# Optimization experiments

Measured on AMD Instinct MI355X. Metric: run time of the kernel, lower is better.

The kernel has to match this reference:

```python
import jax, jax.numpy as jnp
import numpy as np

# Dimensions (match init_kwargs / input_specs)
N = 50000      # num_nodes
R = 16         # num_relations
B = 8          # num_bases
DIN = 128      # indim
DOUT = 128     # outdim
NNZ = 1_600_000  # nonzeros in block-sparse relational adjacency A (N x R*N)


def setup_inputs() -> dict:
    key = jax.random.key(0)
    k0, k1, k2, k3, k4, k5 = jax.random.split(key, 6)
    X = jax.random.normal(k0, (N, DIN), dtype=jnp.float32)
    # COO representation of sparse A: rows in [0, N), cols in [0, R*N)
    A_rows = jax.random.randint(k1, (NNZ,), 0, N, dtype=jnp.int64)
    A_cols = jax.random.randint(k2, (NNZ,), 0, R * N, dtype=jnp.int64)
    A_vals = jax.random.uniform(k3, (NNZ,), dtype=jnp.float32)
    # Basis-decomposed relation weights (xavier-ish scale)
    weight_F = jax.random.normal(k4, (B, DIN, DOUT), dtype=jnp.float32) * 0.05
    weight_F_comp = jax.random.normal(k5, (R, B), dtype=jnp.float32) * 0.3
    return {"X": X, "A_rows": A_rows, "A_cols": A_cols, "A_vals": A_vals,
            "weight_F": weight_F, "weight_F_comp": weight_F_comp}


def reference(X, A_rows, A_cols, A_vals, weight_F, weight_F_comp):
    # Basis decomposition: per-relation weights W_F[r] = sum_b comp[r,b] * basis[b]
    W_F = jnp.einsum('rb,bij->rij', weight_F_comp, weight_F)          # (R, DIN, DOUT)
    # Per-relation feature transform: X @ W_F[r] for all r
    FW_F = jnp.einsum('nj,rjk->rnk', X, W_F)                          # (R, N, DOUT)
    FW_F = FW_F.reshape(R * N, DOUT)                                  # (R*N, DOUT)
    # Sparse-dense matmul A @ FW_F via gather + weighted segment-sum
    gathered = A_vals[:, None] * FW_F[A_cols]                          # (NNZ, DOUT)
    AFW_F = jax.ops.segment_sum(gathered, A_rows, num_segments=N)     # (N, DOUT)
    return AFW_F
```

## Files before the change

### kernel.cpp

```cpp
#include <hip/hip_runtime.h>

typedef unsigned int   uint32;
typedef unsigned short ushort16;

#define NN       50000
#define RR       16
#define BB       8
#define DIN      128
#define DOUT     128
#define K2       1024
#define NNZ_C    1600000
#define NBUCK    196
#define EPB      4096
#define NBLK_E   391

typedef short  short8  __attribute__((ext_vector_type(8)));
typedef float  floatx4 __attribute__((ext_vector_type(4)));
typedef float  float2v __attribute__((ext_vector_type(2)));

__device__ __forceinline__ ushort16 f2bf(float f) {
    uint32 u = __float_as_uint(f);
    u += 0x7fffu + ((u >> 16) & 1u);
    return (ushort16)(u >> 16);
}

__device__ __forceinline__ float bf2f(ushort16 h) {
    return __uint_as_float(((uint32)h) << 16);
}

__device__ __forceinline__ uint32 pack_bf16(float a, float b) {
    uint32 ua = __float_as_uint(a) + 0x8000u;
    uint32 ub = __float_as_uint(b) + 0x8000u;
    return __builtin_amdgcn_perm(ub, ua, 0x07060302);
}

__device__ __forceinline__ void gload16(const void* g, void* l) {
    __builtin_amdgcn_global_load_lds(
        (const __attribute__((address_space(1))) uint32*)g,
        (__attribute__((address_space(3))) uint32*)l, 16, 0, 0);
}

__global__ void build_bst_kernel(const float* __restrict__ basis,
                                 ushort16* __restrict__ Bst) {
    int idx  = blockIdx.x * 256 + threadIdx.x;
    int jout = idx >> 10;
    int bk   = idx & 1023;
    Bst[idx] = f2bf(basis[(size_t)bk * DOUT + jout]);
}

__global__ void cvt_x_kernel(const float* __restrict__ X,
                             uint32* __restrict__ XD) {
    int d = blockIdx.x * 256 + threadIdx.x;
    float2 f = *(const float2*)(X + (size_t)d * 2);
    XD[d] = pack_bf16(f.x, f.y);
}

__global__ void histB_kernel(const int* __restrict__ rows,
                             int* __restrict__ counts) {
    __shared__ int h[NBUCK];
    int tid = threadIdx.x;
    if (tid < NBUCK) h[tid] = 0;
    __syncthreads();
    int base_e = blockIdx.x * EPB;
#pragma unroll
    for (int it = 0; it < 16; ++it) {
        int e = base_e + it * 256 + tid;
        if (e < NNZ_C) atomicAdd(&h[rows[e] >> 8], 1);
    }
    __syncthreads();
    if (tid < NBUCK && h[tid]) atomicAdd(&counts[tid], h[tid]);
}

__global__ void scanB_kernel(const int* __restrict__ counts,
                             int* __restrict__ bucket_start,
                             int* __restrict__ cursor) {
    __shared__ int tmp[256];
    int tid = threadIdx.x;
    int v = (tid < NBUCK) ? counts[tid] : 0;
    tmp[tid] = v;
    __syncthreads();
#pragma unroll
    for (int off = 1; off < 256; off <<= 1) {
        int t = (tid >= off) ? tmp[tid - off] : 0;
        __syncthreads();
        tmp[tid] += t;
        __syncthreads();
    }
    if (tid < NBUCK) {
        bucket_start[tid + 1] = tmp[tid];
        cursor[tid] = tmp[tid] - v;
        if (tid == 0) bucket_start[0] = 0;
    }
}

__global__ __launch_bounds__(256) void scatterB_kernel(
        const int* __restrict__ rows,
        const int* __restrict__ cols,
        const float* __restrict__ vals,
        int* __restrict__ cursor,
        uint2* __restrict__ es2) {
    __shared__ int h[NBUCK], gbase[NBUCK], lcur[NBUCK];
    int tid = threadIdx.x;
    if (tid < NBUCK) { h[tid] = 0; lcur[tid] = 0; }
    __syncthreads();

    int    rowv[16];
    uint32 pkx[16];
    float  vv[16];
    int base_e = blockIdx.x * EPB;
#pragma unroll
    for (int it = 0; it < 16; ++it) {
        int e = base_e + it * 256 + tid;
        if (e < NNZ_C) {
            int row = rows[e];
            int col = cols[e];
            int r   = (int)((uint32)col / (uint32)NN);
            int c   = col - r * NN;
            rowv[it] = row;
            pkx[it]  = (uint32)c | ((uint32)(((row & 255) << 4) | r) << 16);
            vv[it]   = vals[e];
            atomicAdd(&h[row >> 8], 1);
        } else rowv[it] = -1;
    }
    __syncthreads();
    if (tid < NBUCK && h[tid] > 0)
        gbase[tid] = atomicAdd(&cursor[tid], h[tid]);
    __syncthreads();
#pragma unroll
    for (int it = 0; it < 16; ++it) {
        if (rowv[it] >= 0) {
            int b   = rowv[it] >> 8;
            int pos = gbase[b] + atomicAdd(&lcur[b], 1);
            es2[pos] = make_uint2(pkx[it], __float_as_uint(vv[it]));
        }
    }
}

__global__ __launch_bounds__(256) void sortB_kernel(
        const uint2* __restrict__ es2,
        const int* __restrict__ bucket_start,
        uint2* __restrict__ es,
        int* __restrict__ ks) {
    __shared__ int h[4096];
    __shared__ int cur[4096];
    __shared__ int tmp[256];
    int b    = blockIdx.x;
    int tid  = threadIdx.x;
    int base = bucket_start[b];
    int n    = bucket_start[b + 1] - base;

#pragma unroll
    for (int j = 0; j < 16; ++j) h[j * 256 + tid] = 0;
    __syncthreads();
    for (int i = tid; i < n; i += 256) {
        uint2 p = es2[base + i];
        atomicAdd(&h[(p.x >> 16) & 0xfffu], 1);
    }
    __syncthreads();

    int run = 0;
    int loc[16];
#pragma unroll
    for (int j = 0; j < 16; ++j) {
        int c = h[tid * 16 + j];
        loc[j] = run;
        run += c;
    }
    tmp[tid] = run;
    __syncthreads();
#pragma unroll
    for (int off = 1; off < 256; off <<= 1) {
        int t = (tid >= off) ? tmp[tid - off] : 0;
        __syncthreads();
        tmp[tid] += t;
        __syncthreads();
    }
    int excl_t = tmp[tid] - run;
#pragma unroll
    for (int j = 0; j < 16; ++j) {
        int idx = tid * 16 + j;
        int st  = loc[j] + excl_t;
        cur[idx] = st;
        ks[b * 4096 + idx] = base + st;
    }
    __syncthreads();

    for (int i = tid; i < n; i += 256) {
        uint2 p  = es2[base + i];
        int   kl = (p.x >> 16) & 0xfffu;
        int  pos = atomicAdd(&cur[kl], 1);
        es[base + pos] = make_uint2((p.x & 0xffffu) | ((uint32)(kl & 15) << 16),
                                    p.y);
    }
}

__global__ __launch_bounds__(256) void zc_build_kernel(
        const uint2* __restrict__ es,
        const int* __restrict__ ks,
        const uint32* __restrict__ XD,
        const float* __restrict__ comp,
        uint32* __restrict__ ZD) {
    __shared__ __align__(16) float comp_l[128];
    int tid = threadIdx.x;
    if (tid < 128) comp_l[tid] = comp[tid];
    __syncthreads();

    const int row  = __builtin_amdgcn_readfirstlane(blockIdx.x * 4 + (tid >> 6));
    const int lane = tid & 63;

    int beg = __builtin_amdgcn_readfirstlane(ks[row * 16]);
    int end = __builtin_amdgcn_readfirstlane(ks[row * 16 + 16]);

    float2v zb[8];
#pragma unroll
    for (int b = 0; b < 8; ++b) zb[b] = (float2v){0.f, 0.f};

    if (beg < end) {
        const int endm1 = end - 1;
        float2v a = (float2v){0.f, 0.f};

#define LREC(C, R, V, IDX)                                                 \
        { int i_ = (IDX) < endm1 ? (IDX) : endm1;                          \
          uint2 pz_ = es[i_];                                              \
          uint32 px_ = __builtin_amdgcn_readfirstlane(pz_.x);              \
          V = __uint_as_float(__builtin_amdgcn_readfirstlane(pz_.y));      \
          C = (int)(px_ & 0xffffu); R = (int)(px_ >> 16); }

#define LX(X, C)  X = XD[((size_t)(C) << 6) + lane];

#define FOLD                                                               \
        { float4 c0_ = *(const float4*)&comp_l[r_cur * 8];                 \
          float4 c1_ = *(const float4*)&comp_l[r_cur * 8 + 4];             \
          zb[0] += c0_.x * a; zb[1] += c0_.y * a;                          \
          zb[2] += c0_.z * a; zb[3] += c0_.w * a;                          \
          zb[4] += c1_.x * a; zb[5] += c1_.y * a;                          \
          zb[6] += c1_.z * a; zb[7] += c1_.w * a; }

#define CONS(R, V, X, K)                                                   \
        if (e + (K) < end) {                                               \
            if ((R) != r_cur) {                                            \
                FOLD                                                       \
                a = (float2v){0.f, 0.f};                                   \
                r_cur = (R);                                               \
            }                                                              \
            float2v xf_;                                                   \
            xf_.x = __uint_as_float((X) << 16);                            \
            xf_.y = __uint_as_float((X) & 0xffff0000u);                    \
            a += (V) * xf_;                                                \
        }

        int   cA0, cA1, cA2, cA3, rA0, rA1, rA2, rA3;
        int   cB0, cB1, cB2, cB3, rB0, rB1, rB2, rB3;
        float vA0, vA1, vA2, vA3, vB0, vB1, vB2, vB3;
        uint32 xA0, xA1, xA2, xA3;

        LREC(cA0, rA0, vA0, beg + 0)
        LREC(cA1, rA1, vA1, beg + 1)
        LREC(cA2, rA2, vA2, beg + 2)
        LREC(cA3, rA3, vA3, beg + 3)
        LREC(cB0, rB0, vB0, beg + 4)
        LREC(cB1, rB1, vB1, beg + 5)
        LREC(cB2, rB2, vB2, beg + 6)
        LREC(cB3, rB3, vB3, beg + 7)
        LX(xA0, cA0) LX(xA1, cA1) LX(xA2, cA2) LX(xA3, cA3)

        int r_cur = rA0;

        for (int e = beg; e < end; e += 8) {
            uint32 xB0, xB1, xB2, xB3;
            LX(xB0, cB0) LX(xB1, cB1) LX(xB2, cB2) LX(xB3, cB3)
            int cC0, cC1, cC2, cC3, rC0, rC1, rC2, rC3;
            float vC0, vC1, vC2, vC3;
            LREC(cC0, rC0, vC0, e + 8)
            LREC(cC1, rC1, vC1, e + 9)
            LREC(cC2, rC2, vC2, e + 10)
            LREC(cC3, rC3, vC3, e + 11)

            CONS(rA0, vA0, xA0, 0)
            CONS(rA1, vA1, xA1, 1)
            CONS(rA2, vA2, xA2, 2)
            CONS(rA3, vA3, xA3, 3)

            uint32 xC0, xC1, xC2, xC3;
            LX(xC0, cC0) LX(xC1, cC1) LX(xC2, cC2) LX(xC3, cC3)
            int cD0, cD1, cD2, cD3, rD0, rD1, rD2, rD3;
            float vD0, vD1, vD2, vD3;
            LREC(cD0, rD0, vD0, e + 12)
            LREC(cD1, rD1, vD1, e + 13)
            LREC(cD2, rD2, vD2, e + 14)
            LREC(cD3, rD3, vD3, e + 15)

            CONS(rB0, vB0, xB0, 4)
            CONS(rB1, vB1, xB1, 5)
            CONS(rB2, vB2, xB2, 6)
            CONS(rB3, vB3, xB3, 7)

            cA0 = cC0; cA1 = cC1; cA2 = cC2; cA3 = cC3;
            rA0 = rC0; rA1 = rC1; rA2 = rC2; rA3 = rC3;
            vA0 = vC0; vA1 = vC1; vA2 = vC2; vA3 = vC3;
            xA0 = xC0; xA1 = xC1; xA2 = xC2; xA3 = xC3;
            cB0 = cD0; cB1 = cD1; cB2 = cD2; cB3 = cD3;
            rB0 = rD0; rB1 = rD1; rB2 = rD2; rB3 = rD3;
            vB0 = vD0; vB1 = vD1; vB2 = vD2; vB3 = vD3;
        }
        FOLD
#undef CONS
#undef FOLD
#undef LX
#undef LREC
    }

#pragma unroll
    for (int b = 0; b < 8; ++b)
        ZD[(size_t)row * 512 + b * 64 + lane] = pack_bf16(zb[b].x, zb[b].y);
}

__global__ __launch_bounds__(256) void gemm_out_kernel(
        const ushort16* __restrict__ Zc,
        const ushort16* __restrict__ Bst,
        float* __restrict__ out) {
    __shared__ __align__(16) char lds[32768];
    char* Al = lds;
    char* Bl = lds + 16384;

    const int tid  = threadIdx.x;
    const int wave = tid >> 6;
    const int lane = tid & 63;
    const int m    = lane & 15;
    const int half = lane >> 4;
    const int wr   = wave >> 1;
    const int wc   = wave & 1;
    const size_t arow0 = (size_t)blockIdx.x * 128;

    floatx4 acc[16] = {};

    for (int slab = 0; slab < 16; ++slab) {
        const int k0 = slab * 64;
#pragma unroll
        for (int rd = 0; rd < 4; ++rd) {
            int s   = rd * 256 + wave * 64 + lane;
            int row = s >> 3;
            int kc  = (s & 7) ^ (row & 7);
            size_t ldsoff = (size_t)(rd * 256 + wave * 64) * 16;
            gload16(Zc  + ((arow0 + row) << 10) + k0 + (kc << 3), Al + ldsoff);
            gload16(Bst + ((size_t)row << 10)   + k0 + (kc << 3), Bl + ldsoff);
        }
        __syncthreads();

#pragma unroll
        for (int c = 0; c < 2; ++c) {
            short8 a[4], bfr[4];
#pragma unroll
            for (int mt = 0; mt < 4; ++mt) {
                int row = wr * 64 + mt * 16 + m;
                int p   = row * 8 + ((c * 4 + half) ^ (m & 7));
                a[mt] = *(const short8*)(Al + p * 16);
            }
#pragma unroll
            for (int nt = 0; nt < 4; ++nt) {
                int rowb = wc * 64 + nt * 16 + m;
                int p    = rowb * 8 + ((c * 4 + half) ^ (m & 7));
                bfr[nt] = *(const short8*)(Bl + p * 16);
            }
#pragma unroll
            for (int mt = 0; mt < 4; ++mt)
#pragma unroll
                for (int nt = 0; nt < 4; ++nt)
                    acc[mt * 4 + nt] = __builtin_amdgcn_mfma_f32_16x16x32_bf16(
                        a[mt], bfr[nt], acc[mt * 4 + nt], 0, 0, 0);
        }
        __syncthreads();
    }

#pragma unroll
    for (int mt = 0; mt < 4; ++mt) {
#pragma unroll
        for (int reg = 0; reg < 4; ++reg) {
            int grow = (int)arow0 + wr * 64 + mt * 16 + half * 4 + reg;
            if (grow < NN) {
#pragma unroll
                for (int nt = 0; nt < 4; ++nt)
                    out[(size_t)grow * DOUT + wc * 64 + nt * 16 + m] =
                        acc[mt * 4 + nt][reg];
            }
        }
    }
}

extern "C" void kernel_launch(void* const* d_in, const int* in_sizes, int n_in,
                              void* d_out, int out_size, void* d_ws, size_t ws_size,
                              hipStream_t stream) {
    const float* X      = (const float*)d_in[0];
    const int*   A_rows = (const int*)d_in[1];
    const int*   A_cols = (const int*)d_in[2];
    const float* A_vals = (const float*)d_in[3];
    const float* basis  = (const float*)d_in[4];
    const float* comp   = (const float*)d_in[5];
    float* out = (float*)d_out;

    char* ws = (char*)d_ws;
    ushort16* Bst          = (ushort16*)(ws + 0);
    uint32*   XD           = (uint32*)(ws + 524288);
    int*      ks           = (int*)(ws + 13324288);
    uint2*    es           = (uint2*)(ws + 16535552);
    int*      bucket_start = (int*)(ws + 29335552);
    int*      counts       = (int*)(ws + 29336576);
    int*      cursor       = (int*)(ws + 29337600);
    uint2*    es2          = (uint2*)(ws + 29339648);
    ushort16* Zc           = (ushort16*)(ws + 42139648);
    uint32*   ZD           = (uint32*)Zc;

    hipMemsetAsync(counts, 0, NBUCK * sizeof(int), stream);

    build_bst_kernel<<<512, 256, 0, stream>>>(basis, Bst);
    cvt_x_kernel<<<12500, 256, 0, stream>>>(X, XD);

    histB_kernel<<<NBLK_E, 256, 0, stream>>>(A_rows, counts);
    scanB_kernel<<<1, 256, 0, stream>>>(counts, bucket_start, cursor);
    scatterB_kernel<<<NBLK_E, 256, 0, stream>>>(A_rows, A_cols, A_vals,
                                                cursor, es2);
    sortB_kernel<<<NBUCK, 256, 0, stream>>>(es2, bucket_start, es, ks);

    zc_build_kernel<<<12500, 256, 0, stream>>>(es, ks, XD, comp, ZD);

    gemm_out_kernel<<<(NN + 127) / 128, 256, 0, stream>>>(Zc, Bst, out);
}
```

Measured before the change: 254.2 us.

## Replace two-level bucket sort with direct per-key global counting sort and packed FMAs

The preprocessing changes from a bucket-then-local sort to a direct global counting sort over (row, relation) keys. It uses global-atomic histograms, a two-pass multi-block scan and a global-atomic scatter, which removes the intermediate es2 buffer and the sortB pass. The zc_build inner loop is unrolled to 16 edges with four rotating register sets, which removes the register-copy shuffles. It also uses inline v_pk_fma_f32 for the value scaling and the basis fold, with comp values duplicated in LDS. The cost is many global atomics over 800K counters, an extra 3.2 MB memset, and the loss of edge order within a key, which makes float summation order nondeterministic.

```diff
diff --git a/kernel.cpp b/kernel.cpp
--- a/kernel.cpp
+++ b/kernel.cpp
@@ -10,22 +10,20 @@
 #define DOUT     128
 #define K2       1024
 #define NNZ_C    1600000
-#define NBUCK    196
+#define NKEY     800000
 #define EPB      4096
 #define NBLK_E   391
+#define NBLK_K   196
 
 typedef short  short8  __attribute__((ext_vector_type(8)));
 typedef float  floatx4 __attribute__((ext_vector_type(4)));
 typedef float  float2v __attribute__((ext_vector_type(2)));
+typedef uint32 uint2v  __attribute__((ext_vector_type(2)));
 
 __device__ __forceinline__ ushort16 f2bf(float f) {
     uint32 u = __float_as_uint(f);
     u += 0x7fffu + ((u >> 16) & 1u);
     return (ushort16)(u >> 16);
-}
-
-__device__ __forceinline__ float bf2f(ushort16 h) {
-    return __uint_as_float(((uint32)h) << 16);
 }
 
 __device__ __forceinline__ uint32 pack_bf16(float a, float b) {
@@ -55,28 +53,60 @@
     XD[d] = pack_bf16(f.x, f.y);
 }
 
-__global__ void histB_kernel(const int* __restrict__ rows,
-                             int* __restrict__ counts) {
-    __shared__ int h[NBUCK];
+__global__ void histK_kernel(const int* __restrict__ rows,
+                             const int* __restrict__ cols,
+                             int* __restrict__ cnt) {
     int tid = threadIdx.x;
-    if (tid < NBUCK) h[tid] = 0;
-    __syncthreads();
     int base_e = blockIdx.x * EPB;
 #pragma unroll
     for (int it = 0; it < 16; ++it) {
         int e = base_e + it * 256 + tid;
-        if (e < NNZ_C) atomicAdd(&h[rows[e] >> 8], 1);
-    }
+        if (e < NNZ_C) {
+            int r = (int)((uint32)cols[e] / (uint32)NN);
+            atomicAdd(&cnt[rows[e] * 16 + r], 1);
+        }
+    }
+}
+
+__global__ __launch_bounds__(256) void scan1_kernel(const int* __restrict__ cnt,
+                                                    int* __restrict__ ks,
+                                                    int* __restrict__ bsum) {
+    __shared__ int tmp[256];
+    int b = blockIdx.x, tid = threadIdx.x;
+    int j0 = b * 4096 + tid * 16;
+    int v[16];
+    int run = 0;
+#pragma unroll
+    for (int k = 0; k < 16; ++k) {
+        int j = j0 + k;
+        int c = (j < NKEY) ? cnt[j] : 0;
+        v[k] = run;
+        run += c;
+    }
+    tmp[tid] = run;
     __syncthreads();
-    if (tid < NBUCK && h[tid]) atomicAdd(&counts[tid], h[tid]);
-}
-
-__global__ void scanB_kernel(const int* __restrict__ counts,
-                             int* __restrict__ bucket_start,
-                             int* __restrict__ cursor) {
+#pragma unroll
+    for (int off = 1; off < 256; off <<= 1) {
+        int t = (tid >= off) ? tmp[tid - off] : 0;
+        __syncthreads();
+        tmp[tid] += t;
+        __syncthreads();
+    }
+    int excl = tmp[tid] - run;
+#pragma unroll
+    for (int k = 0; k < 16; ++k) {
+        int j = j0 + k;
+        if (j < NKEY) ks[j] = v[k] + excl;
+    }
+    if (tid == 255) bsum[b] = tmp[255];
+}
+
+__global__ __launch_bounds__(256) void scan2_kernel(const int* __restrict__ bsum,
+                                                    int* __restrict__ ks,
+                                                    int* __restrict__ cursor) {
     __shared__ int tmp[256];
-    int tid = threadIdx.x;
-    int v = (tid < NBUCK) ? counts[tid] : 0;
+    int b = blockIdx.x, tid = threadIdx.x;
+    int v = (tid < b) ? bsum[tid] : 0;
     tmp[tid] = v;
     __syncthreads();
 #pragma unroll
@@ -86,28 +116,31 @@
         tmp[tid] += t;
         __syncthreads();
     }
-    if (tid < NBUCK) {
-        bucket_start[tid + 1] = tmp[tid];
-        cursor[tid] = tmp[tid] - v;
-        if (tid == 0) bucket_start[0] = 0;
-    }
-}
-
-__global__ __launch_bounds__(256) void scatterB_kernel(
+    int off_b = tmp[255];
+    int j0 = b * 4096 + tid * 16;
+#pragma unroll
+    for (int k = 0; k < 16; ++k) {
+        int j = j0 + k;
+        if (j < NKEY) {
+            int s = ks[j] + off_b;
+            ks[j] = s;
+            cursor[j] = s;
+        }
+    }
+    if (b == 0 && tid == 0) ks[NKEY] = NNZ_C;
+}
+
+__global__ __launch_bounds__(256) void scatterK_kernel(
         const int* __restrict__ rows,
         const int* __restrict__ cols,
         const float* __restrict__ vals,
         int* __restrict__ cursor,
-        uint2* __restrict__ es2) {
-    __shared__ int h[NBUCK], gbase[NBUCK], lcur[NBUCK];
+        uint2* __restrict__ es) {
     int tid = threadIdx.x;
-    if (tid < NBUCK) { h[tid] = 0; lcur[tid] = 0; }
-    __syncthreads();
-
-    int    rowv[16];
-    uint32 pkx[16];
+    int base_e = blockIdx.x * EPB;
+    int    key[16];
+    uint32 pk[16];
     float  vv[16];
-    int base_e = blockIdx.x * EPB;
 #pragma unroll
     for (int it = 0; it < 16; ++it) {
         int e = base_e + it * 256 + tid;
@@ -116,81 +149,17 @@
             int col = cols[e];
             int r   = (int)((uint32)col / (uint32)NN);
             int c   = col - r * NN;
-            rowv[it] = row;
-            pkx[it]  = (uint32)c | ((uint32)(((row & 255) << 4) | r) << 16);
-            vv[it]   = vals[e];
-            atomicAdd(&h[row >> 8], 1);
-        } else rowv[it] = -1;
-    }
-    __syncthreads();
-    if (tid < NBUCK && h[tid] > 0)
-        gbase[tid] = atomicAdd(&cursor[tid], h[tid]);
-    __syncthreads();
+            key[it] = row * 16 + r;
+            pk[it]  = (uint32)c | ((uint32)r << 16);
+            vv[it]  = vals[e];
+        } else key[it] = -1;
+    }
 #pragma unroll
     for (int it = 0; it < 16; ++it) {
-        if (rowv[it] >= 0) {
-            int b   = rowv[it] >> 8;
-            int pos = gbase[b] + atomicAdd(&lcur[b], 1);
-            es2[pos] = make_uint2(pkx[it], __float_as_uint(vv[it]));
-        }
-    }
-}
-
-__global__ __launch_bounds__(256) void sortB_kernel(
-        const uint2* __restrict__ es2,
-        const int* __restrict__ bucket_start,
-        uint2* __restrict__ es,
-        int* __restrict__ ks) {
-    __shared__ int h[4096];
-    __shared__ int cur[4096];
-    __shared__ int tmp[256];
-    int b    = blockIdx.x;
-    int tid  = threadIdx.x;
-    int base = bucket_start[b];
-    int n    = bucket_start[b + 1] - base;
-
-#pragma unroll
-    for (int j = 0; j < 16; ++j) h[j * 256 + tid] = 0;
-    __syncthreads();
-    for (int i = tid; i < n; i += 256) {
-        uint2 p = es2[base + i];
-        atomicAdd(&h[(p.x >> 16) & 0xfffu], 1);
-    }
-    __syncthreads();
-
-    int run = 0;
-    int loc[16];
-#pragma unroll
-    for (int j = 0; j < 16; ++j) {
-        int c = h[tid * 16 + j];
-        loc[j] = run;
-        run += c;
-    }
-    tmp[tid] = run;
-    __syncthreads();
-#pragma unroll
-    for (int off = 1; off < 256; off <<= 1) {
-        int t = (tid >= off) ? tmp[tid - off] : 0;
-        __syncthreads();
-        tmp[tid] += t;
-        __syncthreads();
-    }
-    int excl_t = tmp[tid] - run;
-#pragma unroll
-    for (int j = 0; j < 16; ++j) {
-        int idx = tid * 16 + j;
-        int st  = loc[j] + excl_t;
-        cur[idx] = st;
-        ks[b * 4096 + idx] = base + st;
-    }
-    __syncthreads();
-
-    for (int i = tid; i < n; i += 256) {
-        uint2 p  = es2[base + i];
-        int   kl = (p.x >> 16) & 0xfffu;
-        int  pos = atomicAdd(&cur[kl], 1);
-        es[base + pos] = make_uint2((p.x & 0xffffu) | ((uint32)(kl & 15) << 16),
-                                    p.y);
+        if (key[it] >= 0) {
+            int pos = atomicAdd(&cursor[key[it]], 1);
+            es[pos] = make_uint2(pk[it], __float_as_uint(vv[it]));
+        }
     }
 }
 
@@ -200,9 +169,13 @@
         const uint32* __restrict__ XD,
         const float* __restrict__ comp,
         uint32* __restrict__ ZD) {
-    __shared__ __align__(16) float comp_l[128];
+    __shared__ __align__(16) float cl2[256];
     int tid = threadIdx.x;
-    if (tid < 128) comp_l[tid] = comp[tid];
+    if (tid < 128) {
+        float c = comp[tid];
+        cl2[tid * 2]     = c;
+        cl2[tid * 2 + 1] = c;
+    }
     __syncthreads();
 
     const int row  = __builtin_amdgcn_readfirstlane(blockIdx.x * 4 + (tid >> 6));
@@ -219,24 +192,24 @@
         const int endm1 = end - 1;
         float2v a = (float2v){0.f, 0.f};
 
-#define LREC(C, R, V, IDX)                                                 \
+#define LREC(C, R, P, IDX)                                                 \
         { int i_ = (IDX) < endm1 ? (IDX) : endm1;                          \
-          uint2 pz_ = es[i_];                                              \
-          uint32 px_ = __builtin_amdgcn_readfirstlane(pz_.x);              \
-          V = __uint_as_float(__builtin_amdgcn_readfirstlane(pz_.y));      \
+          P = *(const uint2v*)(es + i_);                                   \
+          uint32 px_ = __builtin_amdgcn_readfirstlane(P.x);                \
           C = (int)(px_ & 0xffffu); R = (int)(px_ >> 16); }
 
 #define LX(X, C)  X = XD[((size_t)(C) << 6) + lane];
 
 #define FOLD                                                               \
-        { float4 c0_ = *(const float4*)&comp_l[r_cur * 8];                 \
-          float4 c1_ = *(const float4*)&comp_l[r_cur * 8 + 4];             \
-          zb[0] += c0_.x * a; zb[1] += c0_.y * a;                          \
-          zb[2] += c0_.z * a; zb[3] += c0_.w * a;                          \
-          zb[4] += c1_.x * a; zb[5] += c1_.y * a;                          \
-          zb[6] += c1_.z * a; zb[7] += c1_.w * a; }
-
-#define CONS(R, V, X, K)                                                   \
+        { const float2v* cp_ = (const float2v*)(cl2 + r_cur * 16);         \
+          _Pragma("unroll")                                                \
+          for (int b_ = 0; b_ < 8; ++b_) {                                 \
+              float2v c_ = cp_[b_];                                        \
+              asm("v_pk_fma_f32 %0, %1, %2, %0"                            \
+                  : "+v"(zb[b_]) : "v"(c_), "v"(a));                       \
+          } }
+
+#define CONS(R, P, X, K)                                                   \
         if (e + (K) < end) {                                               \
             if ((R) != r_cur) {                                            \
                 FOLD                                                       \
@@ -246,62 +219,75 @@
             float2v xf_;                                                   \
             xf_.x = __uint_as_float((X) << 16);                            \
             xf_.y = __uint_as_float((X) & 0xffff0000u);                    \
-            a += (V) * xf_;                                                \
-        }
-
-        int   cA0, cA1, cA2, cA3, rA0, rA1, rA2, rA3;
-        int   cB0, cB1, cB2, cB3, rB0, rB1, rB2, rB3;
-        float vA0, vA1, vA2, vA3, vB0, vB1, vB2, vB3;
-        uint32 xA0, xA1, xA2, xA3;
-
-        LREC(cA0, rA0, vA0, beg + 0)
-        LREC(cA1, rA1, vA1, beg + 1)
-        LREC(cA2, rA2, vA2, beg + 2)
-        LREC(cA3, rA3, vA3, beg + 3)
-        LREC(cB0, rB0, vB0, beg + 4)
-        LREC(cB1, rB1, vB1, beg + 5)
-        LREC(cB2, rB2, vB2, beg + 6)
-        LREC(cB3, rB3, vB3, beg + 7)
+            asm("v_pk_fma_f32 %0, %1, %2, %0 op_sel:[0,1,0] op_sel_hi:[1,1,1]" \
+                : "+v"(a) : "v"(xf_), "v"(P));                             \
+        }
+
+        int    cA0, cA1, cA2, cA3, rA0, rA1, rA2, rA3;
+        int    cB0, cB1, cB2, cB3, rB0, rB1, rB2, rB3;
+        int    cC0, cC1, cC2, cC3, rC0, rC1, rC2, rC3;
+        int    cD0, cD1, cD2, cD3, rD0, rD1, rD2, rD3;
+        uint2v pA0, pA1, pA2, pA3, pB0, pB1, pB2, pB3;
+        uint2v pC0, pC1, pC2, pC3, pD0, pD1, pD2, pD3;
+        uint32 xA0, xA1, xA2, xA3, xB0, xB1, xB2, xB3;
+        uint32 xC0, xC1, xC2, xC3, xD0, xD1, xD2, xD3;
+
+        LREC(cA0, rA0, pA0, beg + 0)
+        LREC(cA1, rA1, pA1, beg + 1)
+        LREC(cA2, rA2, pA2, beg + 2)
+        LREC(cA3, rA3, pA3, beg + 3)
+        LREC(cB0, rB0, pB0, beg + 4)
+        LREC(cB1, rB1, pB1, beg + 5)
+        LREC(cB2, rB2, pB2, beg + 6)
+        LREC(cB3, rB3, pB3, beg + 7)
         LX(xA0, cA0) LX(xA1, cA1) LX(xA2, cA2) LX(xA3, cA3)
 
         int r_cur = rA0;
 
-        for (int e = beg; e < end; e += 8) {
-            uint32 xB0, xB1, xB2, xB3;
+        for (int e = beg; e < end; e += 16) {
             LX(xB0, cB0) LX(xB1, cB1) LX(xB2, cB2) LX(xB3, cB3)
-            int cC0, cC1, cC2, cC3, rC0, rC1, rC2, rC3;
-            float vC0, vC1, vC2, vC3;
-            LREC(cC0, rC0, vC0, e + 8)
-            LREC(cC1, rC1, vC1, e + 9)
-            LREC(cC2, rC2, vC2, e + 10)
-            LREC(cC3, rC3, vC3, e + 11)
-
-            CONS(rA0, vA0, xA0, 0)
-            CONS(rA1, vA1, xA1, 1)
-            CONS(rA2, vA2, xA2, 2)
-            CONS(rA3, vA3, xA3, 3)
-
-            uint32 xC0, xC1, xC2, xC3;
+            LREC(cC0, rC0, pC0, e + 8)
+            LREC(cC1, rC1, pC1, e + 9)
+            LREC(cC2, rC2, pC2, e + 10)
+            LREC(cC3, rC3, pC3, e + 11)
+
+            CONS(rA0, pA0, xA0, 0)
+            CONS(rA1, pA1, xA1, 1)
+            CONS(rA2, pA2, xA2, 2)
+            CONS(rA3, pA3, xA3, 3)
+
             LX(xC0, cC0) LX(xC1, cC1) LX(xC2, cC2) LX(xC3, cC3)
-            int cD0, cD1, cD2, cD3, rD0, rD1, rD2, rD3;
-            float vD0, vD1, vD2, vD3;
-            LREC(cD0, rD0, vD0, e + 12)
-            LREC(cD1, rD1, vD1, e + 13)
-            LREC(cD2, rD2, vD2, e + 14)
-            LREC(cD3, rD3, vD3, e + 15)
-
-            CONS(rB0, vB0, xB0, 4)
-            CONS(rB1, vB1, xB1, 5)
-            CONS(rB2, vB2, xB2, 6)
-            CONS(rB3, vB3, xB3, 7)
-
-            cA0 = cC0; cA1 = cC1; cA2 = cC2; cA3 = cC3;
-            rA0 = rC0; rA1 = rC1; rA2 = rC2; rA3 = rC3;
-            vA0 = vC0; vA1 = vC1; vA2 = vC2; vA3 = vC3;
-            xA0 = xC0; xA1 = xC1; xA2 = xC2; xA3 = xC3;
-            cB0 = cD0; cB1 = cD1; cB2 = cD2; cB3 = cD3;
-            rB0 = rD0; rB1 = rD1; rB2 = rD2; rB3 = rD3;
-            vB0 = vD0; vB1 = vD1; vB2 = vD2; vB3 = vD3;
+            LREC(cD0, rD0, pD0, e + 12)
+            LREC(cD1, rD1, pD1, e + 13)
+            LREC(cD2, rD2, pD2, e + 14)
+            LREC(cD3, rD3, pD3, e + 15)
+
+            CONS(rB0, pB0, xB0, 4)
+            CONS(rB1, pB1, xB1, 5)
+            CONS(rB2, pB2, xB2, 6)
+            CONS(rB3, pB3, xB3, 7)
+
+            LX(xD0, cD0) LX(xD1, cD1) LX(xD2, cD2) LX(xD3, cD3)
+            LREC(cA0, rA0, pA0, e + 16)
+            LREC(cA1, rA1, pA1, e + 17)
+            LREC(cA2, rA2, pA2, e + 18)
+            LREC(cA3, rA3, pA3, e + 19)
+
+            CONS(rC0, pC0, xC0, 8)
+            CONS(rC1, pC1, xC1, 9)
+            CONS(rC2, pC2, xC2, 10)
+            CONS(rC3, pC3, xC3, 11)
+
+            LX(xA0, cA0) LX(xA1, cA1) LX(xA2, cA2) LX(xA3, cA3)
+            LREC(cB0, rB0, pB0, e + 20)
+            LREC(cB1, rB1, pB1, e + 21)
+            LREC(cB2, rB2, pB2, e + 22)
+            LREC(cB3, rB3, pB3, e + 23)
+
+            CONS(rD0, pD0, xD0, 12)
+            CONS(rD1, pD1, xD1, 13)
+            CONS(rD2, pD2, xD2, 14)
+            CONS(rD3, pD3, xD3, 15)
         }
         FOLD
 #undef CONS
@@ -399,27 +385,25 @@
     float* out = (float*)d_out;
 
     char* ws = (char*)d_ws;
-    ushort16* Bst          = (ushort16*)(ws + 0);
-    uint32*   XD           = (uint32*)(ws + 524288);
-    int*      ks           = (int*)(ws + 13324288);
-    uint2*    es           = (uint2*)(ws + 16535552);
-    int*      bucket_start = (int*)(ws + 29335552);
-    int*      counts       = (int*)(ws + 29336576);
-    int*      cursor       = (int*)(ws + 29337600);
-    uint2*    es2          = (uint2*)(ws + 29339648);
-    ushort16* Zc           = (ushort16*)(ws + 42139648);
-    uint32*   ZD           = (uint32*)Zc;
-
-    hipMemsetAsync(counts, 0, NBUCK * sizeof(int), stream);
+    ushort16* Bst    = (ushort16*)(ws + 0);
+    uint32*   XD     = (uint32*)(ws + 262144);
+    int*      ks     = (int*)(ws + 13062400);
+    int*      cursor = (int*)(ws + 16262656);
+    int*      bsum   = (int*)(ws + 19462912);
+    uint2*    es     = (uint2*)(ws + 19464192);
+    ushort16* Zc     = (ushort16*)(ws + 32264448);
+    uint32*   ZD     = (uint32*)Zc;
+
+    hipMemsetAsync(cursor, 0, NKEY * sizeof(int), stream);
 
     build_bst_kernel<<<512, 256, 0, stream>>>(basis, Bst);
     cvt_x_kernel<<<12500, 256, 0, stream>>>(X, XD);
 
-    histB_kernel<<<NBLK_E, 256, 0, stream>>>(A_rows, counts);
-    scanB_kernel<<<1, 256, 0, stream>>>(counts, bucket_start, cursor);
-    scatterB_kernel<<<NBLK_E, 256, 0, stream>>>(A_rows, A_cols, A_vals,
-                                                cursor, es2);
-    sortB_kernel<<<NBUCK, 256, 0, stream>>>(es2, bucket_start, es, ks);
+    histK_kernel<<<NBLK_E, 256, 0, stream>>>(A_rows, A_cols, cursor);
+    scan1_kernel<<<NBLK_K, 256, 0, stream>>>(cursor, ks, bsum);
+    scan2_kernel<<<NBLK_K, 256, 0, stream>>>(bsum, ks, cursor);
+    scatterK_kernel<<<NBLK_E, 256, 0, stream>>>(A_rows, A_cols, A_vals,
+                                                cursor, es);
 
     zc_build_kernel<<<12500, 256, 0, stream>>>(es, ks, XD, comp, ZD);
 
```

Result: slower. 394.3 us (+55.1%).
